# Optimization experiments

Hardware: AMD Instinct MI355X
Metric: run time of the kernel (lower is better)

The kernel has to match this reference:

```python
import jax, jax.numpy as jnp
import numpy as np

B, N, C = 16, 577, 768
H = 12
D = C // H
HID = C // 2
TEMP_MIN, TEMP_MAX = 0.5, 3.0


def setup_inputs() -> dict:
    key = jax.random.key(0)
    ks = jax.random.split(key, 8)
    s = 0.02
    return {
        "x": jax.random.normal(ks[0], (B, N, C), dtype=jnp.float32),
        "qkv_w": jax.random.normal(ks[1], (C, 3 * C), dtype=jnp.float32) * s,
        "proj_w": jax.random.normal(ks[2], (C, C), dtype=jnp.float32) * s,
        "proj_b": jnp.zeros((C,), dtype=jnp.float32),
        "t_w1": jax.random.normal(ks[3], (C, HID), dtype=jnp.float32) * s,
        "t_b1": jnp.zeros((HID,), dtype=jnp.float32),
        "t_w2": jax.random.normal(ks[4], (HID, 1), dtype=jnp.float32) * s,
        "t_b2": jnp.zeros((1,), dtype=jnp.float32),
    }


def reference(x, qkv_w, proj_w, proj_b, t_w1, t_b1, t_w2, t_b2):
    b, n, c = x.shape
    scale = D ** -0.5
    # instance-wise temperature from CLS token: (B, 1)
    cls = x[:, 0]
    h = jax.nn.relu(cls @ t_w1 + t_b1)
    t_norm = jax.nn.sigmoid(h @ t_w2 + t_b2)
    temperature = TEMP_MIN + (TEMP_MAX - TEMP_MIN) * t_norm  # (B, 1)

    qkv = (x @ qkv_w).reshape(b, n, 3, H, D)
    q = qkv[:, :, 0].transpose(0, 2, 1, 3)  # (B, H, N, D)
    k = qkv[:, :, 1].transpose(0, 2, 1, 3)
    v = qkv[:, :, 2].transpose(0, 2, 1, 3)

    attn = jnp.einsum('bhqd,bhkd->bhqk', q, k) * scale
    attn = attn / temperature[:, :, None, None]  # (B,1,1,1) broadcast
    attn = jax.nn.softmax(attn, axis=-1)
    out = jnp.einsum('bhqk,bhkd->bhqd', attn, v)
    out = out.transpose(0, 2, 1, 3).reshape(b, n, c)
    return out @ proj_w + proj_b
```

## Files before the change

kernel.cpp:

```cpp
#include <hip/hip_runtime.h>
#include <hip/hip_bf16.h>
#include <stdint.h>

typedef unsigned short u16;
typedef unsigned int   u32;
typedef uint64_t       u64;

using f32x4  = __attribute__((ext_vector_type(4))) float;
using bf16x8 = __attribute__((ext_vector_type(8))) short;

__device__ __forceinline__ u16 f2bf(float f){
  u32 x = __builtin_bit_cast(u32, f);
  x = x + 0x7fffu + ((x >> 16) & 1u);
  return (u16)(x >> 16);
}

__device__ __forceinline__ void gload16(const void* g, void* l){
  __builtin_amdgcn_global_load_lds(
      (const __attribute__((address_space(1))) void*)g,
      (__attribute__((address_space(3))) void*)l, 16, 0, 0);
}

__device__ __forceinline__ bf16x8 mkfrag(uint2 h0, uint2 h1){
  union { bf16x8 v; u32 u[4]; } f;
  f.u[0]=h0.x; f.u[1]=h0.y; f.u[2]=h1.x; f.u[3]=h1.y;
  return f.v;
}

__global__ void convx(const float* __restrict__ in, u16* __restrict__ out, int n4){
  for (int i = blockIdx.x*256 + threadIdx.x; i < n4; i += gridDim.x*256){
    float4 v = ((const float4*)in)[i];
    ushort4 o;
    o.x = f2bf(v.x); o.y = f2bf(v.y); o.z = f2bf(v.z); o.w = f2bf(v.w);
    ((ushort4*)out)[i] = o;
  }
}

__global__ __launch_bounds__(256) void wtrans(const float* __restrict__ in,
                                              u16* __restrict__ out, int K, int N){
  __shared__ float tile[32][33];
  const int t = threadIdx.x;
  const int n0 = blockIdx.x*32, k0 = blockIdx.y*32;
  const int r = t >> 3, c4 = (t & 7)*4;
  const float4 v = *(const float4*)(in + (u64)(k0 + r)*N + n0 + c4);
  tile[r][c4+0]=v.x; tile[r][c4+1]=v.y; tile[r][c4+2]=v.z; tile[r][c4+3]=v.w;
  __syncthreads();
  ushort4 o;
  o.x = f2bf(tile[c4+0][r]); o.y = f2bf(tile[c4+1][r]);
  o.z = f2bf(tile[c4+2][r]); o.w = f2bf(tile[c4+3][r]);
  *(ushort4*)(out + (u64)(n0 + r)*K + k0 + c4) = o;
}

__global__ __launch_bounds__(384) void temp_kernel(
    const float* __restrict__ x, const float* __restrict__ w1,
    const float* __restrict__ b1, const float* __restrict__ w2,
    const float* __restrict__ b2, float* __restrict__ lsc){
  const int b = blockIdx.x, t = threadIdx.x;
  __shared__ float cls[768];
  __shared__ float part[6];
  const float* xr = x + (u64)b*577*768;
  cls[t] = xr[t]; cls[t+384] = xr[t+384];
  __syncthreads();
  float h0 = 0.f, h1 = 0.f, h2 = 0.f, h3 = 0.f;
  for (int i = 0; i < 768; i += 4){
    h0 = fmaf(cls[i+0], w1[(u64)(i+0)*384 + t], h0);
    h1 = fmaf(cls[i+1], w1[(u64)(i+1)*384 + t], h1);
    h2 = fmaf(cls[i+2], w1[(u64)(i+2)*384 + t], h2);
    h3 = fmaf(cls[i+3], w1[(u64)(i+3)*384 + t], h3);
  }
  float hacc = fmaxf((h0 + h1) + (h2 + h3) + b1[t], 0.f);
  float v = hacc * w2[t];
  #pragma unroll
  for (int off = 1; off < 64; off <<= 1) v += __shfl_xor(v, off);
  if ((t & 63) == 0) part[t >> 6] = v;
  __syncthreads();
  if (t == 0){
    float s2 = b2[0];
    for (int i = 0; i < 6; i++) s2 += part[i];
    float sig  = 1.f / (1.f + expf(-s2));
    float temp = 0.5f + 2.5f * sig;
    lsc[b] = 0.125f / temp;
  }
}

template<int OUTF>
__global__ __launch_bounds__(256, 2) void gemm_nt(
    const u16* __restrict__ A, const u16* __restrict__ Bm,
    void* __restrict__ Cout, const float* __restrict__ bias,
    const float* __restrict__ lsc, int M, int N){
  constexpr int K = 768;
  __shared__ u16 As[128*64];
  __shared__ u16 Bs[128*64];
  const int t = threadIdx.x, l = t & 63, w = t >> 6;
  const int bm = blockIdx.y*128, bn = blockIdx.x*128;
  const int wr = (w >> 1)*64, wc = (w & 1)*64;
  const int g = l >> 4, r16 = l & 15;

  f32x4 acc[4][4];
  #pragma unroll
  for (int i = 0; i < 4; i++)
    #pragma unroll
    for (int j = 0; j < 4; j++) acc[i][j] = (f32x4){0.f,0.f,0.f,0.f};

  const int srow = t >> 3;
  const int su   = (t & 7) ^ (srow & 7);
  const u16* gA[4]; const u16* gB[4];
  #pragma unroll
  for (int i = 0; i < 4; i++){
    int ra = bm + i*32 + srow; if (ra > M-1) ra = M-1;
    gA[i] = A  + (u64)ra*K + su*8;
    gB[i] = Bm + (u64)(bn + i*32 + srow)*K + su*8;
  }
  u16* lA = As + t*8;
  u16* lB = Bs + t*8;

  for (int kt = 0; kt < K; kt += 64){
    #pragma unroll
    for (int i = 0; i < 4; i++) gload16(gA[i] + kt, lA + i*2048);
    #pragma unroll
    for (int i = 0; i < 4; i++) gload16(gB[i] + kt, lB + i*2048);
    __syncthreads();
    #pragma unroll
    for (int s = 0; s < 2; s++){
      const int c   = s*4 + (g >> 1);
      const int off = (g & 1)*4;
      bf16x8 af[4], bfr[4];
      #pragma unroll
      for (int m = 0; m < 4; m++){
        const int R = wr + m*16 + r16;
        const int i1 = R*64 + ((c ^ (R & 7))*8) + off;
        af[m] = mkfrag(*(const uint2*)(As + i1), *(const uint2*)(As + (i1 ^ 16)));
      }
      #pragma unroll
      for (int n = 0; n < 4; n++){
        const int R = wc + n*16 + r16;
        const int i1 = R*64 + ((c ^ (R & 7))*8) + off;
        bfr[n] = mkfrag(*(const uint2*)(Bs + i1), *(const uint2*)(Bs + (i1 ^ 16)));
      }
      #pragma unroll
      for (int m = 0; m < 4; m++)
        #pragma unroll
        for (int n = 0; n < 4; n++)
          acc[m][n] = __builtin_amdgcn_mfma_f32_16x16x32_bf16(af[m], bfr[n], acc[m][n], 0, 0, 0);
    }
    __syncthreads();
  }
  const int row0 = bm + wr + g*4;
  const int col0 = bn + wc + r16;
  const bool isQ = (OUTF == 2) && (bn < 768);
  #pragma unroll
  for (int m = 0; m < 4; m++){
    #pragma unroll
    for (int rr = 0; rr < 4; rr++){
      const int row = row0 + m*16 + rr;
      if (row < M){
        float qs = 1.0f;
        if (isQ) qs = lsc[row/577];
        #pragma unroll
        for (int n = 0; n < 4; n++){
          const int col = col0 + n*16;
          const float v = acc[m][n][rr];
          if (OUTF == 1) ((float*)Cout)[(u64)row*N + col] = v + bias[col];
          else           ((u16*)Cout)[(u64)row*N + col]  = f2bf(v*qs);
        }
      }
    }
  }
}

__global__ __launch_bounds__(256, 2) void attn_kernel(
    const u16* __restrict__ qkv, u16* __restrict__ aout){
  const int qt = blockIdx.x, h = blockIdx.y, b = blockIdx.z;
  const int t = threadIdx.x, w = t >> 6, l = t & 63;
  const int g = l >> 4, r16 = l & 15;
  __shared__ u16 Ks[2][64*64];
  __shared__ u16 Vt[2][64*64];
  const u16* base = qkv + (u64)b*577*2304 + (u64)h*64;

  int qn = qt*64 + w*16 + r16; if (qn > 576) qn = 576;
  bf16x8 qf[2];
  {
    const u16* qr = base + (u64)qn*2304;
    #pragma unroll
    for (int s = 0; s < 2; s++)
      qf[s] = mkfrag(*(const uint2*)(qr + s*32 + g*4),
                     *(const uint2*)(qr + s*32 + g*4 + 16));
  }
  float m_run = -1e30f, l_run = 0.f;
  f32x4 oacc[4];
  #pragma unroll
  for (int i = 0; i < 4; i++) oacc[i] = (f32x4){0,0,0,0};

  const int srcb = (l & 48) | (((l >> 4) & 3)*4);

  const int srow = t >> 3;
  const int su   = (t & 7) ^ (srow & 7);
  const u16* pK = base + 768  + (u64)srow*2304 + su*8;
  const int kr0 = (t >> 3)*2;
  const u16* pV = base + 1536 + (u64)kr0*2304 + (t & 7)*8;
  u32 vtoff[8];
  #pragma unroll
  for (int j = 0; j < 8; j++){
    const int d = (t & 7)*8 + j;
    const int key = (d ^ (d >> 3)) & 7;
    vtoff[j] = d*64 + (((kr0 >> 3) ^ key)*8) + (kr0 & 7);
  }

  uint4 vr0, vr1;
  gload16(pK,            &Ks[0][0] + t*8);
  gload16(pK + 32*2304,  &Ks[0][0] + t*8 + 2048);
  vr0 = *(const uint4*)pV;
  vr1 = *(const uint4*)(pV + 2304);
  pK += 64*2304; pV += 64*2304;
  {
    const u16* e0 = (const u16*)&vr0;
    const u16* e1 = (const u16*)&vr1;
    #pragma unroll
    for (int j = 0; j < 8; j++)
      *(u32*)(&Vt[0][0] + vtoff[j]) = (u32)e0[j] | ((u32)e1[j] << 16);
  }
  __syncthreads();

  for (int kt = 0; kt < 10; kt++){
    const int cur = kt & 1, nb = cur ^ 1;
    u16* ksc = &Ks[cur][0];
    u16* vtc = &Vt[cur][0];
    if (kt < 9){
      gload16(pK,           &Ks[nb][0] + t*8);
      gload16(pK + 32*2304, &Ks[nb][0] + t*8 + 2048);
      vr0 = *(const uint4*)pV;
      vr1 = *(const uint4*)(pV + 2304);
      pK += 64*2304; pV += 64*2304;
    }

    f32x4 sacc[4];
    #pragma unroll
    for (int i = 0; i < 4; i++) sacc[i] = (f32x4){0,0,0,0};
    #pragma unroll
    for (int fn = 0; fn < 4; fn++){
      const int kr = fn*16 + r16;
      const int kk = kr & 7;
      const u16* rowp = ksc + kr*64 + (g & 1)*4;
      #pragma unroll
      for (int s = 0; s < 2; s++){
        const int b0 = (4*s + (g >> 1)) ^ kk;
        sacc[fn] = __builtin_amdgcn_mfma_f32_16x16x32_bf16(
            mkfrag(*(const uint2*)(rowp + b0*8), *(const uint2*)(rowp + (b0 ^ 2)*8)),
            qf[s], sacc[fn], 0, 0, 0);
      }
    }
    if (kt == 9){
      #pragma unroll
      for (int fn = 0; fn < 4; fn++)
        #pragma unroll
        for (int rr = 0; rr < 4; rr++){
          const bool valid = (576 + fn*16 + g*4 + rr) <= 576;
          sacc[fn][rr] = valid ? sacc[fn][rr] : -1e30f;
        }
    }
    float mx = sacc[0][0];
    #pragma unroll
    for (int fn = 0; fn < 4; fn++)
      #pragma unroll
      for (int rr = 0; rr < 4; rr++) mx = fmaxf(mx, sacc[fn][rr]);
    mx = fmaxf(mx, __shfl_xor(mx, 16));
    mx = fmaxf(mx, __shfl_xor(mx, 32));
    const float nm = fmaxf(m_run, mx);
    const float corr = __expf(m_run - nm);
    m_run = nm;
    float rs = 0.f;
    u16 pb[4][4];
    #pragma unroll
    for (int fn = 0; fn < 4; fn++)
      #pragma unroll
      for (int rr = 0; rr < 4; rr++){
        const float p = __expf(sacc[fn][rr] - m_run);
        rs += p;
        pb[fn][rr] = f2bf(p);
      }
    rs += __shfl_xor(rs, 16);
    rs += __shfl_xor(rs, 32);
    l_run = l_run*corr + rs;
    float corrO[4];
    #pragma unroll
    for (int rr = 0; rr < 4; rr++) corrO[rr] = __shfl(corr, srcb + rr);
    #pragma unroll
    for (int df = 0; df < 4; df++)
      #pragma unroll
      for (int rr = 0; rr < 4; rr++)
        oacc[df][rr] *= corrO[rr];
    #pragma unroll
    for (int s = 0; s < 2; s++){
      union { bf16x8 v; u32 u[4]; } pa;
      pa.u[0] = (u32)pb[2*s][0]   | ((u32)pb[2*s][1]   << 16);
      pa.u[1] = (u32)pb[2*s][2]   | ((u32)pb[2*s][3]   << 16);
      pa.u[2] = (u32)pb[2*s+1][0] | ((u32)pb[2*s+1][1] << 16);
      pa.u[3] = (u32)pb[2*s+1][2] | ((u32)pb[2*s+1][3] << 16);
      #pragma unroll
      for (int df = 0; df < 4; df++){
        const int vd = df*16 + r16;
        const int vk = (vd ^ (vd >> 3)) & 7;
        const u16* vrp = vtc + vd*64 + (g & 1)*4;
        const int c0 = (4*s + (g >> 1)) ^ vk;
        const bf16x8 vf = mkfrag(*(const uint2*)(vrp + c0*8),
                                 *(const uint2*)(vrp + (c0 ^ 2)*8));
        oacc[df] = __builtin_amdgcn_mfma_f32_16x16x32_bf16(pa.v, vf, oacc[df], 0, 0, 0);
      }
    }
    if (kt < 9){
      const u16* e0 = (const u16*)&vr0;
      const u16* e1 = (const u16*)&vr1;
      u16* vtn = &Vt[nb][0];
      #pragma unroll
      for (int j = 0; j < 8; j++)
        *(u32*)(vtn + vtoff[j]) = (u32)e0[j] | ((u32)e1[j] << 16);
    }
    __syncthreads();
  }
  float lO[4];
  #pragma unroll
  for (int rr = 0; rr < 4; rr++) lO[rr] = __shfl(l_run, srcb + rr);
  #pragma unroll
  for (int df = 0; df < 4; df++){
    const int d = df*16 + r16;
    #pragma unroll
    for (int rr = 0; rr < 4; rr++){
      const int n = qt*64 + w*16 + g*4 + rr;
      if (n <= 576){
        const float v = oacc[df][rr] / lO[rr];
        aout[(u64)(b*577 + n)*768 + h*64 + d] = f2bf(v);
      }
    }
  }
}

extern "C" void kernel_launch(void* const* d_in, const int* in_sizes, int n_in,
                              void* d_out, int out_size, void* d_ws, size_t ws_size,
                              hipStream_t stream){
  const float* x      = (const float*)d_in[0];
  const float* qkv_w  = (const float*)d_in[1];
  const float* proj_w = (const float*)d_in[2];
  const float* proj_b = (const float*)d_in[3];
  const float* t_w1   = (const float*)d_in[4];
  const float* t_b1   = (const float*)d_in[5];
  const float* t_w2   = (const float*)d_in[6];
  const float* t_b2   = (const float*)d_in[7];

  const u64 off_xb  = 256;
  const u64 off_qwT = off_xb  + 14180352ull;
  const u64 off_pwT = off_qwT + 3538944ull;
  const u64 off_qkv = off_pwT + 1179648ull;
  const u64 need    = off_qkv + 42835968ull;
  if (ws_size < need) return;

  char* ws  = (char*)d_ws;
  float* lsc = (float*)ws;
  u16* xb   = (u16*)(ws + off_xb);
  u16* qwT  = (u16*)(ws + off_qwT);
  u16* pwT  = (u16*)(ws + off_pwT);
  u16* qkv  = (u16*)(ws + off_qkv);
  u16* ao   = xb;

  convx<<<1024, 256, 0, stream>>>(x, xb, (16*577*768)/4);
  wtrans<<<dim3(2304/32, 768/32), 256, 0, stream>>>(qkv_w, qwT, 768, 2304);
  wtrans<<<dim3(768/32, 768/32), 256, 0, stream>>>(proj_w, pwT, 768, 768);
  temp_kernel<<<16, 384, 0, stream>>>(x, t_w1, t_b1, t_w2, t_b2, lsc);
  gemm_nt<2><<<dim3(2304/128, 73), 256, 0, stream>>>(xb, qwT, qkv, nullptr, lsc, 9232, 2304);
  attn_kernel<<<dim3(10, 12, 16), 256, 0, stream>>>(qkv, ao);
  gemm_nt<1><<<dim3(768/128, 73), 256, 0, stream>>>(ao, pwT, d_out, proj_b, nullptr, 9232, 768);
}
```

Baseline: 255.1 us.

## Handle tail key scalarly, skip lazy softmax rescale, remap blocks for locality

The attention loop now covers only the nine full 64-key tiles. The single leftover key (index 576) is handled by a scalar dot product and a rank-1 update instead of a mostly masked tenth MFMA tile. The online softmax rescale is skipped unless some row's max grows by more than 8, which bounds exp growth. Blocks are launched on a flat grid with a swizzled mapping so co-resident blocks share heads in cache. P is converted with packed bf16 cvt instructions. The final __syncthreads is dropped, and the workspace requirement shrinks slightly.

```diff
diff --git a/kernel.cpp b/kernel.cpp
--- a/kernel.cpp
+++ b/kernel.cpp
@@ -170,7 +170,12 @@
 
 __global__ __launch_bounds__(256, 2) void attn_kernel(
     const u16* __restrict__ qkv, u16* __restrict__ aout){
-  const int qt = blockIdx.x, h = blockIdx.y, b = blockIdx.z;
+  const u32 lid  = blockIdx.x;
+  const u32 orig = (lid & 7u)*240u + (lid >> 3);
+  const int qt = orig % 10u;
+  const u32 bh = orig / 10u;
+  const int h  = bh % 12u;
+  const int b  = bh / 12u;
   const int t = threadIdx.x, w = t >> 6, l = t & 63;
   const int g = l >> 4, r16 = l & 15;
   __shared__ u16 Ks[2][64*64];
@@ -221,11 +226,11 @@
   }
   __syncthreads();
 
-  for (int kt = 0; kt < 10; kt++){
+  for (int kt = 0; kt < 9; kt++){
     const int cur = kt & 1, nb = cur ^ 1;
     u16* ksc = &Ks[cur][0];
     u16* vtc = &Vt[cur][0];
-    if (kt < 9){
+    if (kt < 8){
       gload16(pK,           &Ks[nb][0] + t*8);
       gload16(pK + 32*2304, &Ks[nb][0] + t*8 + 2048);
       vr0 = *(const uint4*)pV;
@@ -249,15 +254,6 @@
             qf[s], sacc[fn], 0, 0, 0);
       }
     }
-    if (kt == 9){
-      #pragma unroll
-      for (int fn = 0; fn < 4; fn++)
-        #pragma unroll
-        for (int rr = 0; rr < 4; rr++){
-          const bool valid = (576 + fn*16 + g*4 + rr) <= 576;
-          sacc[fn][rr] = valid ? sacc[fn][rr] : -1e30f;
-        }
-    }
     float mx = sacc[0][0];
     #pragma unroll
     for (int fn = 0; fn < 4; fn++)
@@ -265,37 +261,39 @@
       for (int rr = 0; rr < 4; rr++) mx = fmaxf(mx, sacc[fn][rr]);
     mx = fmaxf(mx, __shfl_xor(mx, 16));
     mx = fmaxf(mx, __shfl_xor(mx, 32));
-    const float nm = fmaxf(m_run, mx);
-    const float corr = __expf(m_run - nm);
-    m_run = nm;
+    if (!__all(mx - m_run <= 8.f)){
+      const float nm = fmaxf(m_run, mx);
+      const float corr = __expf(m_run - nm);
+      l_run *= corr;
+      float corrO[4];
+      #pragma unroll
+      for (int rr = 0; rr < 4; rr++) corrO[rr] = __shfl(corr, srcb + rr);
+      #pragma unroll
+      for (int df = 0; df < 4; df++)
+        #pragma unroll
+        for (int rr = 0; rr < 4; rr++) oacc[df][rr] *= corrO[rr];
+      m_run = nm;
+    }
+    float pf[4][4];
     float rs = 0.f;
-    u16 pb[4][4];
     #pragma unroll
     for (int fn = 0; fn < 4; fn++)
       #pragma unroll
       for (int rr = 0; rr < 4; rr++){
         const float p = __expf(sacc[fn][rr] - m_run);
         rs += p;
-        pb[fn][rr] = f2bf(p);
+        pf[fn][rr] = p;
       }
     rs += __shfl_xor(rs, 16);
     rs += __shfl_xor(rs, 32);
-    l_run = l_run*corr + rs;
-    float corrO[4];
-    #pragma unroll
-    for (int rr = 0; rr < 4; rr++) corrO[rr] = __shfl(corr, srcb + rr);
-    #pragma unroll
-    for (int df = 0; df < 4; df++)
-      #pragma unroll
-      for (int rr = 0; rr < 4; rr++)
-        oacc[df][rr] *= corrO[rr];
+    l_run += rs;
     #pragma unroll
     for (int s = 0; s < 2; s++){
       union { bf16x8 v; u32 u[4]; } pa;
-      pa.u[0] = (u32)pb[2*s][0]   | ((u32)pb[2*s][1]   << 16);
-      pa.u[1] = (u32)pb[2*s][2]   | ((u32)pb[2*s][3]   << 16);
-      pa.u[2] = (u32)pb[2*s+1][0] | ((u32)pb[2*s+1][1] << 16);
-      pa.u[3] = (u32)pb[2*s+1][2] | ((u32)pb[2*s+1][3] << 16);
+      asm("v_cvt_pk_bf16_f32 %0, %1, %2" : "=v"(pa.u[0]) : "v"(pf[2*s][0]),   "v"(pf[2*s][1]));
+      asm("v_cvt_pk_bf16_f32 %0, %1, %2" : "=v"(pa.u[1]) : "v"(pf[2*s][2]),   "v"(pf[2*s][3]));
+      asm("v_cvt_pk_bf16_f32 %0, %1, %2" : "=v"(pa.u[2]) : "v"(pf[2*s+1][0]), "v"(pf[2*s+1][1]));
+      asm("v_cvt_pk_bf16_f32 %0, %1, %2" : "=v"(pa.u[3]) : "v"(pf[2*s+1][2]), "v"(pf[2*s+1][3]));
       #pragma unroll
       for (int df = 0; df < 4; df++){
         const int vd = df*16 + r16;
@@ -307,16 +305,66 @@
         oacc[df] = __builtin_amdgcn_mfma_f32_16x16x32_bf16(pa.v, vf, oacc[df], 0, 0, 0);
       }
     }
-    if (kt < 9){
+    if (kt < 8){
       const u16* e0 = (const u16*)&vr0;
       const u16* e1 = (const u16*)&vr1;
       u16* vtn = &Vt[nb][0];
       #pragma unroll
       for (int j = 0; j < 8; j++)
         *(u32*)(vtn + vtoff[j]) = (u32)e0[j] | ((u32)e1[j] << 16);
-    }
-    __syncthreads();
-  }
+      __syncthreads();
+    }
+  }
+
+  {
+    const u16* kr576 = base + 768 + (u64)576*2304;
+    float s576 = 0.f;
+    #pragma unroll
+    for (int s = 0; s < 2; s++){
+      const uint2 k0 = *(const uint2*)(kr576 + s*32 + g*4);
+      const uint2 k1 = *(const uint2*)(kr576 + s*32 + g*4 + 16);
+      union { bf16x8 v; u32 u[4]; } qq; qq.v = qf[s];
+      const u32 ku[4] = {k0.x, k0.y, k1.x, k1.y};
+      #pragma unroll
+      for (int j = 0; j < 4; j++){
+        const float ql = __builtin_bit_cast(float, qq.u[j] << 16);
+        const float qh = __builtin_bit_cast(float, qq.u[j] & 0xffff0000u);
+        const float kl = __builtin_bit_cast(float, ku[j] << 16);
+        const float kh = __builtin_bit_cast(float, ku[j] & 0xffff0000u);
+        s576 = fmaf(ql, kl, s576);
+        s576 = fmaf(qh, kh, s576);
+      }
+    }
+    s576 += __shfl_xor(s576, 16);
+    s576 += __shfl_xor(s576, 32);
+    if (!__all(s576 - m_run <= 8.f)){
+      const float nm = fmaxf(m_run, s576);
+      const float corr = __expf(m_run - nm);
+      l_run *= corr;
+      float corrO[4];
+      #pragma unroll
+      for (int rr = 0; rr < 4; rr++) corrO[rr] = __shfl(corr, srcb + rr);
+      #pragma unroll
+      for (int df = 0; df < 4; df++)
+        #pragma unroll
+        for (int rr = 0; rr < 4; rr++) oacc[df][rr] *= corrO[rr];
+      m_run = nm;
+    }
+    const float p576 = __expf(s576 - m_run);
+    l_run += p576;
+    float pbr[4];
+    #pragma unroll
+    for (int rr = 0; rr < 4; rr++) pbr[rr] = __shfl(p576, srcb + rr);
+    const u16* v576 = base + 1536 + (u64)576*2304;
+    #pragma unroll
+    for (int df = 0; df < 4; df++){
+      const float vv = __builtin_bit_cast(float, (u32)v576[df*16 + r16] << 16);
+      #pragma unroll
+      for (int rr = 0; rr < 4; rr++)
+        oacc[df][rr] = fmaf(pbr[rr], vv, oacc[df][rr]);
+    }
+  }
+
   float lO[4];
   #pragma unroll
   for (int rr = 0; rr < 4; rr++) lO[rr] = __shfl(l_run, srcb + rr);
@@ -350,7 +398,7 @@
   const u64 off_qwT = off_xb  + 14180352ull;
   const u64 off_pwT = off_qwT + 3538944ull;
   const u64 off_qkv = off_pwT + 1179648ull;
-  const u64 need    = off_qkv + 42835968ull;
+  const u64 need    = off_qkv + 42541056ull;
   if (ws_size < need) return;
 
   char* ws  = (char*)d_ws;
@@ -366,6 +414,6 @@
   wtrans<<<dim3(768/32, 768/32), 256, 0, stream>>>(proj_w, pwT, 768, 768);
   temp_kernel<<<16, 384, 0, stream>>>(x, t_w1, t_b1, t_w2, t_b2, lsc);
   gemm_nt<2><<<dim3(2304/128, 73), 256, 0, stream>>>(xb, qwT, qkv, nullptr, lsc, 9232, 2304);
-  attn_kernel<<<dim3(10, 12, 16), 256, 0, stream>>>(qkv, ao);
+  attn_kernel<<<1920, 256, 0, stream>>>(qkv, ao);
   gemm_nt<1><<<dim3(768/128, 73), 256, 0, stream>>>(ao, pwT, d_out, proj_b, nullptr, 9232, 768);
 }
```

Measured after the change: 238.3 us. 6.6% less time.
